# Performance work log

Measured on AMD Instinct MI355X. Metric: run time of the kernel, lower is better.

## Reference

```python
import jax, jax.numpy as jnp
import numpy as np

IN_SHAPE = (8, 8, 8, 8)   # prod = 4096 in_features
OUT_SHAPE = (8, 8, 8, 8)  # prod = 4096 out_features
RANKS = (1, 64, 64, 64, 1)


def mpo2matrix(cores):
    # cores[k]: (r_k, i_k, o_k, r_{k+1}); contract the TT chain over rank axes.
    t = cores[0]
    for c in cores[1:]:
        t = jnp.tensordot(t, c, axes=([-1], [0]))
    # t: (1, i1,o1, i2,o2, i3,o3, i4,o4, 1) -> drop boundary ranks
    n = len(IN_SHAPE)
    io = tuple(d for p in zip(IN_SHAPE, OUT_SHAPE) for d in p)
    t = t.reshape(io)  # (i1,o1,...,in,on)
    perm = tuple(range(1, 2 * n, 2)) + tuple(range(0, 2 * n, 2))  # outputs first
    t = jnp.transpose(t, perm)
    return t.reshape(int(np.prod(OUT_SHAPE)), int(np.prod(IN_SHAPE)))  # (O, I)


def setup_inputs() -> dict:
    key = jax.random.key(0)
    ks = jax.random.split(key, 6)
    scale = 0.05  # keep reconstructed weight well-conditioned
    cores = []
    for i in range(4):
        r0, r1 = RANKS[i], RANKS[i + 1]
        cores.append(scale * jax.random.normal(ks[i], (r0, IN_SHAPE[i], OUT_SHAPE[i], r1), dtype=jnp.float32))
    x = jax.random.normal(ks[4], (8, 2048, 4096), dtype=jnp.float32)
    bias = jnp.zeros((4096,), dtype=jnp.float32)
    return {"x": x, "core0": cores[0], "core1": cores[1], "core2": cores[2], "core3": cores[3], "bias": bias}


def reference(x, core0, core1, core2, core3, bias):
    W = mpo2matrix([core0, core1, core2, core3])  # (O, I)
    res = x.reshape(-1, x.shape[-1])              # (B*S, I)
    out = res @ W.T + bias                        # F.linear
    return out.reshape(x.shape[:-1] + (-1,))
```

## Files before the change

kernel.cpp:

```cpp
#include <hip/hip_runtime.h>
#include <hip/hip_bf16.h>
#include <stdint.h>

typedef unsigned short u16;
typedef __attribute__((ext_vector_type(4))) float f32x4;
typedef __attribute__((ext_vector_type(8))) __bf16 bf16x8;

#define K_DIM 4096

__device__ __forceinline__ u16 f2bf_rne(float f) {
  union { float f; uint32_t u; } v; v.f = f;
  uint32_t u = v.u;
  return (u16)((u + 0x7fffu + ((u >> 16) & 1u)) >> 16);
}

__device__ __forceinline__ void gld_lds16(const u16* g, u16* l) {
  __builtin_amdgcn_global_load_lds((const __attribute__((address_space(1))) void*)g,
                                   (__attribute__((address_space(3))) void*)l,
                                   16, 0, 0);
}

__global__ __launch_bounds__(256) void k_cvt_x(const float* __restrict__ x, u16* __restrict__ xb, int n4) {
  const int stride = gridDim.x * 256;
  for (int i = blockIdx.x * 256 + threadIdx.x; i < n4; i += stride) {
    f32x4 a = ((const f32x4*)x)[i];
    uint2 o;
    o.x = (uint32_t)f2bf_rne(a[0]) | ((uint32_t)f2bf_rne(a[1]) << 16);
    o.y = (uint32_t)f2bf_rne(a[2]) | ((uint32_t)f2bf_rne(a[3]) << 16);
    ((uint2*)xb)[i] = o;
  }
}

__global__ __launch_bounds__(256) void k_t1(const float* __restrict__ c0, const float* __restrict__ c1,
                                            float* __restrict__ T1) {
  const int col = blockIdx.x * 256 + threadIdx.x;
  const int row = blockIdx.y;
  float acc = 0.f;
#pragma unroll 16
  for (int r = 0; r < 64; ++r) acc += c0[row * 64 + r] * c1[(size_t)r * 4096 + col];
  T1[(size_t)row * 4096 + col] = acc;
}

__global__ __launch_bounds__(256) void k_t2(const float* __restrict__ T1, const float* __restrict__ c2,
                                            float* __restrict__ T2) {
  __shared__ float t1s[16][64];
  const int tid = threadIdx.x;
  const int rowbase = blockIdx.y * 16;
  for (int idx = tid; idx < 1024; idx += 256)
    t1s[idx >> 6][idx & 63] = T1[(size_t)(rowbase + (idx >> 6)) * 64 + (idx & 63)];
  __syncthreads();
  const int col = blockIdx.x * 256 + tid;
  float acc[16];
#pragma unroll
  for (int j = 0; j < 16; ++j) acc[j] = 0.f;
  for (int r = 0; r < 64; ++r) {
    float b = c2[(size_t)r * 4096 + col];
#pragma unroll
    for (int j = 0; j < 16; ++j) acc[j] += t1s[j][r] * b;
  }
#pragma unroll
  for (int j = 0; j < 16; ++j) T2[(size_t)(rowbase + j) * 4096 + col] = acc[j];
}

__global__ __launch_bounds__(256) void k_w(const float* __restrict__ T2, const float* __restrict__ c3,
                                           u16* __restrict__ Wb) {
  __shared__ float t2p[64 * 65];
  __shared__ float c3s[64 * 64];
  const int tid = threadIdx.x;
  const int row12 = blockIdx.x;
  for (int idx = tid; idx < 4096; idx += 256) {
    t2p[(idx >> 6) * 65 + (idx & 63)] = T2[(size_t)row12 * 4096 + idx];
    c3s[idx] = c3[idx];
  }
  __syncthreads();
  const int orow = tid >> 2;
  const int o3 = orow >> 3, o4 = orow & 7;
  const int ib16 = (tid & 3) * 16;
  float acc[16];
#pragma unroll
  for (int c = 0; c < 16; ++c) acc[c] = 0.f;
  for (int r3 = 0; r3 < 64; ++r3) {
#pragma unroll
    for (int c = 0; c < 16; ++c) {
      const int i = ib16 + c;
      acc[c] += t2p[((i >> 3) * 8 + o3) * 65 + r3] * c3s[r3 * 64 + (i & 7) * 8 + o4];
    }
  }
  const int i1o1 = row12 >> 6, i2o2 = row12 & 63;
  const int obase = ((i1o1 & 7) << 9) | ((i2o2 & 7) << 6);
  const int ibase = ((i1o1 >> 3) << 9) | ((i2o2 >> 3) << 6);
  uint32_t pk[8];
#pragma unroll
  for (int c = 0; c < 8; ++c)
    pk[c] = (uint32_t)f2bf_rne(acc[2 * c]) | ((uint32_t)f2bf_rne(acc[2 * c + 1]) << 16);
  uint4* dst = (uint4*)&Wb[(size_t)(obase + orow) * 4096 + ibase + ib16];
  dst[0] = make_uint4(pk[0], pk[1], pk[2], pk[3]);
  dst[1] = make_uint4(pk[4], pk[5], pk[6], pk[7]);
}

__global__ __launch_bounds__(512, 2) void k_gemm(const u16* __restrict__ Xb, const u16* __restrict__ Wb,
                                                 const float* __restrict__ bias, float* __restrict__ out) {
  __shared__ alignas(16) u16 Abuf[3][256 * 32];
  __shared__ alignas(16) u16 Bbuf[3][256 * 32];
  const int tid = threadIdx.x;
  const int wid = tid >> 6, l = tid & 63;
  const int bm = blockIdx.x;
  const int bn = blockIdx.y;
  const int wm = wid >> 2, wn = wid & 3;

  const int ach = (l & 3) ^ ((l >> 3) & 3);
  const size_t ag0 = (size_t)(bm * 256 + wid * 16 + (l >> 2)) * K_DIM + ach * 8;
  const size_t ag1 = ag0 + (size_t)128 * K_DIM;
  const size_t bg0 = (size_t)(bn * 256 + wid * 16 + (l >> 2)) * K_DIM + ach * 8;
  const size_t bg1 = bg0 + (size_t)128 * K_DIM;
  const int lst0 = (wid * 16) * 32;
  const int lst1 = (128 + wid * 16) * 32;

  const int rsw = ((l >> 4) ^ ((l >> 1) & 3)) * 8;
  const int arow0 = wm * 128 + (l & 15);
  const int brow0 = wn * 64 + (l & 15);

  f32x4 acc[8][4];
#pragma unroll
  for (int m = 0; m < 8; ++m)
#pragma unroll
    for (int n = 0; n < 4; ++n) acc[m][n] = (f32x4){0.f, 0.f, 0.f, 0.f};

#define GSTAGE(T, SB) do {                                  \
    const int ko_ = (T) * 32;                               \
    gld_lds16(Xb + ag0 + ko_, &Abuf[SB][lst0]);             \
    gld_lds16(Xb + ag1 + ko_, &Abuf[SB][lst1]);             \
    gld_lds16(Wb + bg0 + ko_, &Bbuf[SB][lst0]);             \
    gld_lds16(Wb + bg1 + ko_, &Bbuf[SB][lst1]);             \
  } while (0)

#define COMPUTE(B) do {                                                                   \
    bf16x8 af[8], bfr[4];                                                                 \
    _Pragma("unroll")                                                                     \
    for (int m = 0; m < 8; ++m) af[m] = *(const bf16x8*)&Abuf[B][(arow0 + m * 16) * 32 + rsw]; \
    _Pragma("unroll")                                                                     \
    for (int n = 0; n < 4; ++n) bfr[n] = *(const bf16x8*)&Bbuf[B][(brow0 + n * 16) * 32 + rsw]; \
    __builtin_amdgcn_s_setprio(1);                                                        \
    _Pragma("unroll")                                                                     \
    for (int m = 0; m < 8; ++m)                                                           \
      _Pragma("unroll")                                                                   \
      for (int n = 0; n < 4; ++n)                                                         \
        acc[m][n] = __builtin_amdgcn_mfma_f32_16x16x32_bf16(af[m], bfr[n], acc[m][n], 0, 0, 0); \
    __builtin_amdgcn_s_setprio(0);                                                        \
  } while (0)

#define BOUNDARY4 do { asm volatile("s_waitcnt vmcnt(4)" ::: "memory"); \
    __builtin_amdgcn_s_barrier(); asm volatile("" ::: "memory"); } while (0)
#define BOUNDARY0 do { asm volatile("s_waitcnt vmcnt(0)" ::: "memory"); \
    __builtin_amdgcn_s_barrier(); asm volatile("" ::: "memory"); } while (0)

  GSTAGE(0, 0);
  GSTAGE(1, 1);
  BOUNDARY4;

#pragma unroll 1
  for (int t3 = 0; t3 < 126; t3 += 3) {
    GSTAGE(t3 + 2, 2); COMPUTE(0); BOUNDARY4;
    GSTAGE(t3 + 3, 0); COMPUTE(1); BOUNDARY4;
    GSTAGE(t3 + 4, 1); COMPUTE(2); BOUNDARY4;
  }
  COMPUTE(0);
  BOUNDARY0;
  COMPUTE(1);

  const int orow_base = bm * 256 + wm * 128 + (l >> 4) * 4;
  const int ocol_base = bn * 256 + wn * 64 + (l & 15);
#pragma unroll
  for (int n = 0; n < 4; ++n) {
    const int oc = ocol_base + n * 16;
    const float bv = bias[oc];
#pragma unroll
    for (int m = 0; m < 8; ++m) {
      const int orb = orow_base + m * 16;
#pragma unroll
      for (int j = 0; j < 4; ++j)
        out[(size_t)(orb + j) * 4096 + oc] = acc[m][n][j] + bv;
    }
  }
#undef GSTAGE
#undef COMPUTE
#undef BOUNDARY4
#undef BOUNDARY0
}

extern "C" void kernel_launch(void* const* d_in, const int* in_sizes, int n_in,
                              void* d_out, int out_size, void* d_ws, size_t ws_size,
                              hipStream_t stream) {
  const float* x    = (const float*)d_in[0];
  const float* c0   = (const float*)d_in[1];
  const float* c1   = (const float*)d_in[2];
  const float* c2   = (const float*)d_in[3];
  const float* c3   = (const float*)d_in[4];
  const float* bias = (const float*)d_in[5];
  float* out = (float*)d_out;

  char* ws = (char*)d_ws;
  float* T1 = (float*)ws;
  float* T2 = (float*)(ws + (1u << 20));
  u16*   Wb = (u16*)(ws + (1u << 20) + (64u << 20));
  u16*   Xb = (u16*)(ws + (1u << 20) + (64u << 20) + (32u << 20));

  hipLaunchKernelGGL(k_cvt_x, dim3(2048), dim3(256), 0, stream, x, Xb, 16777216);
  hipLaunchKernelGGL(k_t1,    dim3(16, 64), dim3(256), 0, stream, c0, c1, T1);
  hipLaunchKernelGGL(k_t2,    dim3(16, 256), dim3(256), 0, stream, T1, c2, T2);
  hipLaunchKernelGGL(k_w,     dim3(4096), dim3(256), 0, stream, T2, c3, Wb);
  hipLaunchKernelGGL(k_gemm,  dim3(64, 16), dim3(512), 0, stream, Xb, Wb, bias, out);
}
```

Baseline: 1.065 ms.

## Restructure GEMM into double-buffered K=64 tiles with interleaved quarter-tile compute

The GEMM main loop moves from a triple-buffered K=32 pipeline to a double-buffered K=64 tile. Each tile is split into four quadrant sub-steps, and each sub-step interleaves one quarter of the next tile's global-to-LDS loads with MFMA work on the current tile, using barriers and vmcnt waits. A new XOR swizzle is meant to avoid LDS bank conflicts at the wider row stride. Separately, the W-construction kernel transposes c3 in shared memory so each thread reads contiguous float4 vectors and reuses two t2 scalars, cutting LDS reads. The extra barriers per tile could add synchronization overhead.

```diff
diff --git a/kernel.cpp b/kernel.cpp
--- a/kernel.cpp
+++ b/kernel.cpp
@@ -65,25 +65,35 @@
 __global__ __launch_bounds__(256) void k_w(const float* __restrict__ T2, const float* __restrict__ c3,
                                            u16* __restrict__ Wb) {
   __shared__ float t2p[64 * 65];
-  __shared__ float c3s[64 * 64];
+  __shared__ float c3t[64 * 64];
   const int tid = threadIdx.x;
   const int row12 = blockIdx.x;
   for (int idx = tid; idx < 4096; idx += 256) {
     t2p[(idx >> 6) * 65 + (idx & 63)] = T2[(size_t)row12 * 4096 + idx];
-    c3s[idx] = c3[idx];
+    const int r3 = idx >> 6, orow = idx & 63;
+    c3t[r3 * 64 + ((orow & 7) << 3) + (orow >> 3)] = c3[idx];
   }
   __syncthreads();
   const int orow = tid >> 2;
   const int o3 = orow >> 3, o4 = orow & 7;
   const int ib16 = (tid & 3) * 16;
+  const int rowA = ((ib16 >> 3)) * 8 + o3;
+  const int rowB = ((ib16 >> 3) + 1) * 8 + o3;
   float acc[16];
 #pragma unroll
   for (int c = 0; c < 16; ++c) acc[c] = 0.f;
   for (int r3 = 0; r3 < 64; ++r3) {
-#pragma unroll
-    for (int c = 0; c < 16; ++c) {
-      const int i = ib16 + c;
-      acc[c] += t2p[((i >> 3) * 8 + o3) * 65 + r3] * c3s[r3 * 64 + (i & 7) * 8 + o4];
+    const float ta = t2p[rowA * 65 + r3];
+    const float tb = t2p[rowB * 65 + r3];
+    const float* cv = &c3t[r3 * 64 + o4 * 8];
+    f32x4 c0v = *(const f32x4*)cv;
+    f32x4 c1v = *(const f32x4*)(cv + 4);
+#pragma unroll
+    for (int j = 0; j < 4; ++j) {
+      acc[j]      += ta * c0v[j];
+      acc[4 + j]  += ta * c1v[j];
+      acc[8 + j]  += tb * c0v[j];
+      acc[12 + j] += tb * c1v[j];
     }
   }
   const int i1o1 = row12 >> 6, i2o2 = row12 & 63;
@@ -100,25 +110,26 @@
 
 __global__ __launch_bounds__(512, 2) void k_gemm(const u16* __restrict__ Xb, const u16* __restrict__ Wb,
                                                  const float* __restrict__ bias, float* __restrict__ out) {
-  __shared__ alignas(16) u16 Abuf[3][256 * 32];
-  __shared__ alignas(16) u16 Bbuf[3][256 * 32];
+  __shared__ alignas(16) u16 Abuf[2][256 * 64];
+  __shared__ alignas(16) u16 Bbuf[2][256 * 64];
   const int tid = threadIdx.x;
   const int wid = tid >> 6, l = tid & 63;
   const int bm = blockIdx.x;
   const int bn = blockIdx.y;
   const int wm = wid >> 2, wn = wid & 3;
 
-  const int ach = (l & 3) ^ ((l >> 3) & 3);
-  const size_t ag0 = (size_t)(bm * 256 + wid * 16 + (l >> 2)) * K_DIM + ach * 8;
-  const size_t ag1 = ag0 + (size_t)128 * K_DIM;
-  const size_t bg0 = (size_t)(bn * 256 + wid * 16 + (l >> 2)) * K_DIM + ach * 8;
-  const size_t bg1 = bg0 + (size_t)128 * K_DIM;
-  const int lst0 = (wid * 16) * 32;
-  const int lst1 = (128 + wid * 16) * 32;
-
-  const int rsw = ((l >> 4) ^ ((l >> 1) & 3)) * 8;
-  const int arow0 = wm * 128 + (l & 15);
-  const int brow0 = wn * 64 + (l & 15);
+  const int sch = (l & 7) ^ ((l >> 3) & 7);
+  const int arow_g = 8 * wid + (l >> 3);
+  const int brow_g = (wid >> 2) * 64 + 8 * (wid & 3) + (l >> 3);
+  const u16* AgBase = Xb + (size_t)(bm * 256) * K_DIM + sch * 8;
+  const u16* BgBase = Wb + (size_t)(bn * 256) * K_DIM + sch * 8;
+  const int aldsw = (8 * wid) * 64;
+  const int bldsw = ((wid >> 2) * 64 + 8 * (wid & 3)) * 64;
+
+  const int kc0 = (((l >> 4)) ^ (l & 7)) * 8;
+  const int kc1 = ((4 + (l >> 4)) ^ (l & 7)) * 8;
+  const int aoff = (wm * 128 + (l & 15)) * 64;
+  const int boff = (wn * 64 + (l & 15)) * 64;
 
   f32x4 acc[8][4];
 #pragma unroll
@@ -126,47 +137,59 @@
 #pragma unroll
     for (int n = 0; n < 4; ++n) acc[m][n] = (f32x4){0.f, 0.f, 0.f, 0.f};
 
-#define GSTAGE(T, SB) do {                                  \
-    const int ko_ = (T) * 32;                               \
-    gld_lds16(Xb + ag0 + ko_, &Abuf[SB][lst0]);             \
-    gld_lds16(Xb + ag1 + ko_, &Abuf[SB][lst1]);             \
-    gld_lds16(Wb + bg0 + ko_, &Bbuf[SB][lst0]);             \
-    gld_lds16(Wb + bg1 + ko_, &Bbuf[SB][lst1]);             \
+  bf16x8 a[4][2], b0[2][2], b1[2][2];
+
+#define STAGE_A(T, S, PB) do { const size_t ko_ = (size_t)(T) * 64;                                  \
+    gld_lds16(AgBase + (size_t)((S) * 64 + arow_g) * K_DIM + ko_,        &Abuf[PB][(S) * 4096 + aldsw]);        \
+    gld_lds16(AgBase + (size_t)(128 + (S) * 64 + arow_g) * K_DIM + ko_,  &Abuf[PB][8192 + (S) * 4096 + aldsw]); \
   } while (0)
-
-#define COMPUTE(B) do {                                                                   \
-    bf16x8 af[8], bfr[4];                                                                 \
-    _Pragma("unroll")                                                                     \
-    for (int m = 0; m < 8; ++m) af[m] = *(const bf16x8*)&Abuf[B][(arow0 + m * 16) * 32 + rsw]; \
-    _Pragma("unroll")                                                                     \
-    for (int n = 0; n < 4; ++n) bfr[n] = *(const bf16x8*)&Bbuf[B][(brow0 + n * 16) * 32 + rsw]; \
-    __builtin_amdgcn_s_setprio(1);                                                        \
-    _Pragma("unroll")                                                                     \
-    for (int m = 0; m < 8; ++m)                                                           \
-      _Pragma("unroll")                                                                   \
-      for (int n = 0; n < 4; ++n)                                                         \
-        acc[m][n] = __builtin_amdgcn_mfma_f32_16x16x32_bf16(af[m], bfr[n], acc[m][n], 0, 0, 0); \
-    __builtin_amdgcn_s_setprio(0);                                                        \
+#define STAGE_B(T, S, PB) do { const size_t ko_ = (size_t)(T) * 64;                                  \
+    gld_lds16(BgBase + (size_t)((S) * 32 + brow_g) * K_DIM + ko_,        &Bbuf[PB][(S) * 2048 + bldsw]);        \
+    gld_lds16(BgBase + (size_t)(128 + (S) * 32 + brow_g) * K_DIM + ko_,  &Bbuf[PB][8192 + (S) * 2048 + bldsw]); \
   } while (0)
 
-#define BOUNDARY4 do { asm volatile("s_waitcnt vmcnt(4)" ::: "memory"); \
-    __builtin_amdgcn_s_barrier(); asm volatile("" ::: "memory"); } while (0)
-#define BOUNDARY0 do { asm volatile("s_waitcnt vmcnt(0)" ::: "memory"); \
-    __builtin_amdgcn_s_barrier(); asm volatile("" ::: "memory"); } while (0)
-
-  GSTAGE(0, 0);
-  GSTAGE(1, 1);
-  BOUNDARY4;
+#define LDA(P, MH) do { _Pragma("unroll") for (int mt = 0; mt < 4; ++mt) {       \
+    a[mt][0] = *(const bf16x8*)&Abuf[P][aoff + (MH) * 4096 + mt * 1024 + kc0];   \
+    a[mt][1] = *(const bf16x8*)&Abuf[P][aoff + (MH) * 4096 + mt * 1024 + kc1]; } } while (0)
+#define LDB(BV, P, NH) do { _Pragma("unroll") for (int nt = 0; nt < 2; ++nt) {   \
+    BV[nt][0] = *(const bf16x8*)&Bbuf[P][boff + (NH) * 2048 + nt * 1024 + kc0];  \
+    BV[nt][1] = *(const bf16x8*)&Bbuf[P][boff + (NH) * 2048 + nt * 1024 + kc1]; } } while (0)
+
+#define MM(MB, NB, BV) do { __builtin_amdgcn_s_setprio(1);                                            \
+    _Pragma("unroll") for (int mt = 0; mt < 4; ++mt)                                                  \
+    _Pragma("unroll") for (int nt = 0; nt < 2; ++nt) {                                                \
+      acc[(MB)+mt][(NB)+nt] = __builtin_amdgcn_mfma_f32_16x16x32_bf16(a[mt][0], BV[nt][0], acc[(MB)+mt][(NB)+nt], 0, 0, 0); \
+      acc[(MB)+mt][(NB)+nt] = __builtin_amdgcn_mfma_f32_16x16x32_bf16(a[mt][1], BV[nt][1], acc[(MB)+mt][(NB)+nt], 0, 0, 0); } \
+    __builtin_amdgcn_s_setprio(0); } while (0)
+
+#define FENCE asm volatile("" ::: "memory")
+#define BAR do { FENCE; __builtin_amdgcn_s_barrier(); FENCE; } while (0)
+#define VMW4 asm volatile("s_waitcnt vmcnt(4)" ::: "memory")
+#define VMW2 asm volatile("s_waitcnt vmcnt(2)" ::: "memory")
+#define VMW0 asm volatile("s_waitcnt vmcnt(0)" ::: "memory")
+#define LGKM asm volatile("s_waitcnt lgkmcnt(0)" ::: "memory")
+
+#define TILE(T, P) do {                                                                          \
+    LDA(P, 0); LDB(b0, P, 0); STAGE_A((T) + 1, 0, (P) ^ 1); BAR; LGKM; MM(0, 0, b0); VMW4; BAR;  \
+    LDB(b1, P, 1);            STAGE_B((T) + 1, 0, (P) ^ 1); BAR; LGKM; MM(0, 2, b1); VMW4; BAR;  \
+    LDA(P, 1);                STAGE_B((T) + 1, 1, (P) ^ 1); BAR; LGKM; MM(4, 2, b1); VMW4; BAR;  \
+                              STAGE_A((T) + 1, 1, (P) ^ 1); BAR;       MM(4, 0, b0); VMW4; BAR;  \
+  } while (0)
+
+  STAGE_A(0, 0, 0); STAGE_B(0, 0, 0); STAGE_B(0, 1, 0); STAGE_A(0, 1, 0);
+  VMW4; BAR;
 
 #pragma unroll 1
-  for (int t3 = 0; t3 < 126; t3 += 3) {
-    GSTAGE(t3 + 2, 2); COMPUTE(0); BOUNDARY4;
-    GSTAGE(t3 + 3, 0); COMPUTE(1); BOUNDARY4;
-    GSTAGE(t3 + 4, 1); COMPUTE(2); BOUNDARY4;
-  }
-  COMPUTE(0);
-  BOUNDARY0;
-  COMPUTE(1);
+  for (int t = 0; t < 62; t += 2) {
+    TILE(t, 0);
+    TILE(t + 1, 1);
+  }
+  TILE(62, 0);
+
+  LDA(1, 0); LDB(b0, 1, 0); BAR; LGKM; MM(0, 0, b0); VMW2; BAR;
+  LDB(b1, 1, 1);            BAR; LGKM; MM(0, 2, b1); VMW0; BAR;
+  LDA(1, 1);                BAR; LGKM; MM(4, 2, b1); BAR;
+                                       MM(4, 0, b0);
 
   const int orow_base = bm * 256 + wm * 128 + (l >> 4) * 4;
   const int ocol_base = bn * 256 + wn * 64 + (l & 15);
@@ -182,10 +205,18 @@
         out[(size_t)(orb + j) * 4096 + oc] = acc[m][n][j] + bv;
     }
   }
-#undef GSTAGE
-#undef COMPUTE
-#undef BOUNDARY4
-#undef BOUNDARY0
+#undef STAGE_A
+#undef STAGE_B
+#undef LDA
+#undef LDB
+#undef MM
+#undef FENCE
+#undef BAR
+#undef VMW4
+#undef VMW2
+#undef VMW0
+#undef LGKM
+#undef TILE
 }
 
 extern "C" void kernel_launch(void* const* d_in, const int* in_sizes, int n_in,
```

New measurement: 1.020 ms. 1.04x faster.
